# Kernel optimization log

Measured on AMD Instinct MI355X. Metric: run time of the kernel, lower is better.

## Reference

```python
import jax, jax.numpy as jnp
import numpy as np

B, T, L, H = 16, 16, 512, 768


def setup_inputs() -> dict:
    key = jax.random.key(0)
    k1, k2, k3, k4, k5, k6 = jax.random.split(key, 6)
    hn = jax.random.normal(k1, (B, L, H), dtype=jnp.float32)
    decoder_out = jax.random.normal(k2, (B, L, H), dtype=jnp.float32)
    W1 = jax.random.normal(k3, (H, H), dtype=jnp.float32) * (1.0 / np.sqrt(H))
    W2 = jax.random.normal(k4, (H, H), dtype=jnp.float32) * (1.0 / np.sqrt(H))
    V = jax.random.normal(k5, (H,), dtype=jnp.float32) * (1.0 / np.sqrt(H))
    # Ragged, consistent pointer indices: T monotone segment starts per sample,
    # gold boundary Yindex[b,t] in [Xindex[b,t], L).
    step = L // T  # 32
    Xindex = jnp.broadcast_to(jnp.arange(T, dtype=jnp.int64) * step, (B, T))
    offsets = jax.random.randint(k6, (B, T), 0, step, dtype=jnp.int64)
    Yindex = Xindex + offsets
    lens = jnp.full((B,), L, dtype=jnp.int64)
    return {"hn": hn, "decoder_out": decoder_out, "W1": W1, "W2": W2, "V": V,
            "Xindex": Xindex, "Yindex": Yindex, "lens": lens}


def reference(hn, decoder_out, W1, W2, V, Xindex, Yindex, lens):
    # Faithful batched form of training_decoder + pointerLayer:
    #   for each sample i, step j:
    #     en = hn[i, Xindex[i,j]:lens[i]]            (ragged suffix)
    #     dj = decoder_out[i, Yindex[i,j]]           (cur_dj = decoder_out[cur_groundy])
    #     s  = selu(V @ selu(W1 en + W2 dj))
    #     loss += NLL(log_softmax(s), Yindex[i,j]-Xindex[i,j])
    WE = jnp.einsum('blh,gh->blg', hn, W1)                        # [B,L,H]  nnW1(en)
    dj = jnp.take_along_axis(decoder_out, Yindex[:, :, None], axis=1)  # [B,T,H]
    WD = jnp.einsum('bth,gh->btg', dj, W2)                        # [B,T,H]  nnW2(dj)
    act = jax.nn.selu(WE[:, None, :, :] + WD[:, :, None, :])      # [B,T,L,H]
    scores = jax.nn.selu(jnp.einsum('btlh,h->btl', act, V))       # [B,T,L]
    pos = jnp.arange(hn.shape[1])
    mask = (pos[None, None, :] >= Xindex[:, :, None]) & (pos[None, None, :] < lens[:, None, None])
    neg_inf = jnp.finfo(scores.dtype).min
    masked = jnp.where(mask, scores, neg_inf)
    logp = masked - jax.scipy.special.logsumexp(masked, axis=-1, keepdims=True)
    # logits index (Yindex - Xindex) in the sliced array == global index Yindex
    gold = jnp.take_along_axis(logp, Yindex[:, :, None], axis=-1)[..., 0]  # [B,T]
    return -jnp.mean(gold)
```

## Files before the change

kernel.cpp:

```cpp
#include <hip/hip_runtime.h>
#include <hip/hip_bf16.h>
#include <math.h>

#define SELU_SCALE 1.0507009873554805f
#define SELU_ALPHA 1.6732632423543772f

static constexpr int B_ = 16, T_ = 16, L_ = 512, H_ = 768;

typedef __bf16 bf16x8 __attribute__((ext_vector_type(8)));
typedef __bf16 bf16x4 __attribute__((ext_vector_type(4)));
typedef float  f32x4  __attribute__((ext_vector_type(4)));

__device__ __forceinline__ float bf_lo(unsigned u) { return __uint_as_float(u << 16); }
__device__ __forceinline__ float bf_hi(unsigned u) { return __uint_as_float(u & 0xFFFF0000u); }

__device__ __forceinline__ float selu_core(float x) {
    float e = fmaf(__expf(x), SELU_ALPHA, -SELU_ALPHA);
    return x > 0.0f ? x : e;
}

__device__ __forceinline__ bf16x4 cvt4(float4 f) {
    bf16x4 o;
    o.x = (__bf16)f.x; o.y = (__bf16)f.y; o.z = (__bf16)f.z; o.w = (__bf16)f.w;
    return o;
}

__global__ __launch_bounds__(256) void prep_k(
        const float* __restrict__ w1, const float* __restrict__ w2,
        const float* __restrict__ dec, const int* __restrict__ Yi,
        __bf16* __restrict__ w1b, __bf16* __restrict__ w2b,
        float* __restrict__ djf, float* __restrict__ out) {
    const int NW = H_ * H_ / 4;
    int i = blockIdx.x * 256 + threadIdx.x;
    if (i == 0) out[0] = 0.0f;
    if (i < NW) {
        ((bf16x4*)w1b)[i] = cvt4(((const float4*)w1)[i]);
    } else if (i < 2 * NW) {
        int j = i - NW;
        ((bf16x4*)w2b)[j] = cvt4(((const float4*)w2)[j]);
    } else {
        int j = i - 2 * NW;
        int bt = j / 192, c = j % 192;
        int b = bt >> 4;
        int y = Yi[bt];
        ((float4*)djf)[bt * 192 + c] = ((const float4*)dec)[(b * L_ + y) * 192 + c];
    }
}

__device__ __forceinline__ void load16_lds(const __bf16* g, __bf16* l) {
    __builtin_amdgcn_global_load_lds(
        (const __attribute__((address_space(1))) unsigned int*)g,
        (__attribute__((address_space(3))) unsigned int*)l, 16, 0, 0);
}

__global__ __launch_bounds__(256) void gemm_k(
        const float* __restrict__ hn, const float* __restrict__ djf,
        const __bf16* __restrict__ w1b, const __bf16* __restrict__ w2b,
        __bf16* __restrict__ web, __bf16* __restrict__ wdb) {
    __shared__ __bf16 As[64 * 64];
    __shared__ __bf16 Bs[128 * 64];

    int bx = blockIdx.x;
    const float* Af; const __bf16* Bw; __bf16* C;
    if (bx < 768) { Af = hn; Bw = w1b; C = web; }
    else          { bx -= 768; Af = djf; Bw = w2b; C = wdb; }
    const int m0 = (bx / 6) * 64, n0 = (bx % 6) * 128;

    const int wave = threadIdx.x >> 6;
    const int lane = threadIdx.x & 63;
    const int wm = (wave >> 1) * 32, wn = (wave & 1) * 64;
    const int lr = lane & 15, q = lane >> 4;

    const int ar = threadIdx.x >> 2, asp = threadIdx.x & 3;
    const int s0 = (asp * 2)     ^ (ar & 7);
    const int s1 = (asp * 2 + 1) ^ (ar & 7);
    const float* Ag = Af + (size_t)(m0 + ar) * 768 + asp * 16;
    __bf16* Aw0 = &As[ar * 64 + s0 * 8];
    __bf16* Aw1 = &As[ar * 64 + s1 * 8];

    const int brow = wave * 8 + (lane >> 3);
    const int bcol = ((lane & 7) ^ (lane >> 3)) * 8;
    const __bf16* Bg = Bw + (size_t)(n0 + brow) * 768 + bcol;
    __bf16* Bl = &Bs[(wave * 8) * 64];

    int sl[2];
    sl[0] = ((q)     ^ (lr & 7)) * 8;
    sl[1] = ((4 + q) ^ (lr & 7)) * 8;
    int arow_off[2], brow_off[4];
#pragma unroll
    for (int i = 0; i < 2; ++i) arow_off[i] = (wm + i * 16 + lr) * 64;
#pragma unroll
    for (int j = 0; j < 4; ++j) brow_off[j] = (wn + j * 16 + lr) * 64;

    f32x4 acc[2][4] = {};

    for (int k0 = 0; k0 < 768; k0 += 64) {
#pragma unroll
        for (int c = 0; c < 4; ++c)
            load16_lds(Bg + (size_t)c * 32 * 768 + k0, Bl + c * 32 * 64);
        float4 a0 = *(const float4*)(Ag + k0);
        float4 a1 = *(const float4*)(Ag + k0 + 4);
        float4 a2 = *(const float4*)(Ag + k0 + 8);
        float4 a3 = *(const float4*)(Ag + k0 + 12);
        bf16x8 p0, p1;
        p0[0]=(__bf16)a0.x; p0[1]=(__bf16)a0.y; p0[2]=(__bf16)a0.z; p0[3]=(__bf16)a0.w;
        p0[4]=(__bf16)a1.x; p0[5]=(__bf16)a1.y; p0[6]=(__bf16)a1.z; p0[7]=(__bf16)a1.w;
        p1[0]=(__bf16)a2.x; p1[1]=(__bf16)a2.y; p1[2]=(__bf16)a2.z; p1[3]=(__bf16)a2.w;
        p1[4]=(__bf16)a3.x; p1[5]=(__bf16)a3.y; p1[6]=(__bf16)a3.z; p1[7]=(__bf16)a3.w;
        *(bf16x8*)Aw0 = p0;
        *(bf16x8*)Aw1 = p1;
        __syncthreads();

#pragma unroll
        for (int kc = 0; kc < 2; ++kc) {
            bf16x8 af[2], bfr[4];
#pragma unroll
            for (int i = 0; i < 2; ++i) af[i]  = *(const bf16x8*)&As[arow_off[i] + sl[kc]];
#pragma unroll
            for (int j = 0; j < 4; ++j) bfr[j] = *(const bf16x8*)&Bs[brow_off[j] + sl[kc]];
#pragma unroll
            for (int i = 0; i < 2; ++i)
#pragma unroll
                for (int j = 0; j < 4; ++j)
                    acc[i][j] = __builtin_amdgcn_mfma_f32_16x16x32_bf16(af[i], bfr[j], acc[i][j], 0, 0, 0);
        }
        __syncthreads();
    }

#pragma unroll
    for (int i = 0; i < 2; ++i)
#pragma unroll
        for (int j = 0; j < 4; ++j)
#pragma unroll
            for (int r = 0; r < 4; ++r) {
                int row = m0 + wm + i * 16 + q * 4 + r;
                int col = n0 + wn + j * 16 + lr;
                C[(size_t)row * 768 + col] = (__bf16)acc[i][j][r];
            }
}

__global__ __launch_bounds__(256) void scores_k(
        const __bf16* __restrict__ web, const __bf16* __restrict__ wdb,
        const float* __restrict__ V, const int* __restrict__ Xi,
        float* __restrict__ scores) {
    __shared__ float    we_s[16][772];
    __shared__ unsigned wd_s[16][388];
    __shared__ float    v_s[768];

    const int b = blockIdx.x, l0 = blockIdx.y * 16;

    for (int c = threadIdx.x; c < 16 * 96; c += 256) {
        int r = c / 96, cc = c % 96;
        uint4 v = *(const uint4*)(web + ((size_t)(b * L_ + l0 + r)) * H_ + cc * 8);
        float4 f0, f1;
        f0.x = bf_lo(v.x); f0.y = bf_hi(v.x); f0.z = bf_lo(v.y); f0.w = bf_hi(v.y);
        f1.x = bf_lo(v.z); f1.y = bf_hi(v.z); f1.z = bf_lo(v.w); f1.w = bf_hi(v.w);
        *(float4*)&we_s[r][cc * 8]     = f0;
        *(float4*)&we_s[r][cc * 8 + 4] = f1;
    }
    for (int c = threadIdx.x; c < 16 * 96; c += 256) {
        int r = c / 96, cc = c % 96;
        *(uint4*)&wd_s[r][cc * 4] = *(const uint4*)(wdb + ((size_t)(b * T_ + r)) * H_ + cc * 8);
    }
    if (threadIdx.x < 192) *(float4*)&v_s[threadIdx.x * 4] = ((const float4*)V)[threadIdx.x];
    __syncthreads();

    const int t = threadIdx.x >> 4;
    const int ls = threadIdx.x & 15;
    const int l = l0 + ls;
    const int X = Xi[b * T_ + t];
    if (!__any(l >= X)) return;

    float a0 = 0.f, a1 = 0.f, a2 = 0.f, a3 = 0.f;
#pragma unroll 4
    for (int h = 0; h < H_; h += 8) {
        float4 w0 = *(const float4*)&we_s[ls][h];
        float4 w1 = *(const float4*)&we_s[ls][h + 4];
        uint4  wd = *(const uint4*)&wd_s[t][h >> 1];
        float4 v0 = *(const float4*)&v_s[h];
        float4 v1 = *(const float4*)&v_s[h + 4];
        a0 = fmaf(selu_core(w0.x + bf_lo(wd.x)), v0.x, a0);
        a1 = fmaf(selu_core(w0.y + bf_hi(wd.x)), v0.y, a1);
        a2 = fmaf(selu_core(w0.z + bf_lo(wd.y)), v0.z, a2);
        a3 = fmaf(selu_core(w0.w + bf_hi(wd.y)), v0.w, a3);
        a0 = fmaf(selu_core(w1.x + bf_lo(wd.z)), v1.x, a0);
        a1 = fmaf(selu_core(w1.y + bf_hi(wd.z)), v1.y, a1);
        a2 = fmaf(selu_core(w1.z + bf_lo(wd.w)), v1.z, a2);
        a3 = fmaf(selu_core(w1.w + bf_hi(wd.w)), v1.w, a3);
    }
    float dot = SELU_SCALE * ((a0 + a1) + (a2 + a3));
    float sc  = dot > 0.0f ? SELU_SCALE * dot
                           : SELU_SCALE * SELU_ALPHA * (__expf(dot) - 1.0f);
    scores[((size_t)(b * T_ + t)) * L_ + l] = sc;
}

__global__ __launch_bounds__(64) void loss_k(
        const float* __restrict__ scores, const int* __restrict__ Xi,
        const int* __restrict__ Yi, float* __restrict__ out) {
    const int bt = blockIdx.x;
    const int lane = threadIdx.x;
    const int X = Xi[bt];
    const int Y = Yi[bt];
    const float* row = scores + (size_t)bt * L_;

    float m = -INFINITY;
    for (int l = X + lane; l < L_; l += 64) m = fmaxf(m, row[l]);
#pragma unroll
    for (int off = 32; off > 0; off >>= 1) m = fmaxf(m, __shfl_xor(m, off));

    float s = 0.0f;
    for (int l = X + lane; l < L_; l += 64) s += __expf(row[l] - m);
#pragma unroll
    for (int off = 32; off > 0; off >>= 1) s += __shfl_xor(s, off);

    if (lane == 0)
        atomicAdd(out, (m + __logf(s) - row[Y]) * (1.0f / (B_ * T_)));
}

extern "C" void kernel_launch(void* const* d_in, const int* in_sizes, int n_in,
                              void* d_out, int out_size, void* d_ws, size_t ws_size,
                              hipStream_t stream) {
    const float* hn  = (const float*)d_in[0];
    const float* dec = (const float*)d_in[1];
    const float* W1  = (const float*)d_in[2];
    const float* W2  = (const float*)d_in[3];
    const float* V   = (const float*)d_in[4];
    const int*   Xi  = (const int*)d_in[5];
    const int*   Yi  = (const int*)d_in[6];
    float* out = (float*)d_out;

    char* ws = (char*)d_ws;
    size_t off = 0;
    auto alloc = [&](size_t bytes) -> char* {
        char* p = ws + off;
        off += (bytes + 255) & ~(size_t)255;
        return p;
    };
    __bf16* w1b    = (__bf16*)alloc((size_t)H_ * H_ * 2);
    __bf16* w2b    = (__bf16*)alloc((size_t)H_ * H_ * 2);
    float*  djf    = (float*)alloc((size_t)B_ * T_ * H_ * 4);
    __bf16* web    = (__bf16*)alloc((size_t)B_ * L_ * H_ * 2);
    __bf16* wdb    = (__bf16*)alloc((size_t)B_ * T_ * H_ * 2);
    float*  scores = (float*)alloc((size_t)B_ * T_ * L_ * 4);

    prep_k<<<1344, 256, 0, stream>>>(W1, W2, dec, Yi, w1b, w2b, djf, out);

    gemm_k<<<792, 256, 0, stream>>>(hn, djf, w1b, w2b, web, wdb);

    scores_k<<<dim3(B_, L_ / 16), 256, 0, stream>>>(web, wdb, V, Xi, scores);
    loss_k<<<B_ * T_, 64, 0, stream>>>(scores, Xi, Yi, out);
}
```

Before: 163.6 us.

## Fuse WE GEMM with score computation and split WD GEMM into own kernel

The hn·W1 GEMM is fused into the scores kernel. Each 512-thread block computes a 32×768 WE tile with MFMA, parks it in LDS as bf16, and then evaluates the selu/V reduction for all 16 decoder steps. This removes the global round-trip of the full WE intermediate. The small dj·W2 product moves to its own kernel, fed by bf16 dj from prep. The trade-off is only 256 large blocks with about 78KB of LDS each, so occupancy and parallelism drop, and each block streams all of W1.

```diff
diff --git a/kernel.cpp b/kernel.cpp
--- a/kernel.cpp
+++ b/kernel.cpp
@@ -25,11 +25,19 @@
     return o;
 }
 
+__device__ __forceinline__ int sw3(int r) { return (r ^ (r >> 2)) & 3; }
+
+__device__ __forceinline__ void load16_lds(const __bf16* g, __bf16* l) {
+    __builtin_amdgcn_global_load_lds(
+        (const __attribute__((address_space(1))) unsigned int*)g,
+        (__attribute__((address_space(3))) unsigned int*)l, 16, 0, 0);
+}
+
 __global__ __launch_bounds__(256) void prep_k(
         const float* __restrict__ w1, const float* __restrict__ w2,
         const float* __restrict__ dec, const int* __restrict__ Yi,
         __bf16* __restrict__ w1b, __bf16* __restrict__ w2b,
-        float* __restrict__ djf, float* __restrict__ out) {
+        __bf16* __restrict__ djb, float* __restrict__ out) {
     const int NW = H_ * H_ / 4;
     int i = blockIdx.x * 256 + threadIdx.x;
     if (i == 0) out[0] = 0.0f;
@@ -43,155 +51,147 @@
         int bt = j / 192, c = j % 192;
         int b = bt >> 4;
         int y = Yi[bt];
-        ((float4*)djf)[bt * 192 + c] = ((const float4*)dec)[(b * L_ + y) * 192 + c];
-    }
-}
-
-__device__ __forceinline__ void load16_lds(const __bf16* g, __bf16* l) {
-    __builtin_amdgcn_global_load_lds(
-        (const __attribute__((address_space(1))) unsigned int*)g,
-        (__attribute__((address_space(3))) unsigned int*)l, 16, 0, 0);
-}
-
-__global__ __launch_bounds__(256) void gemm_k(
-        const float* __restrict__ hn, const float* __restrict__ djf,
-        const __bf16* __restrict__ w1b, const __bf16* __restrict__ w2b,
-        __bf16* __restrict__ web, __bf16* __restrict__ wdb) {
-    __shared__ __bf16 As[64 * 64];
-    __shared__ __bf16 Bs[128 * 64];
-
-    int bx = blockIdx.x;
-    const float* Af; const __bf16* Bw; __bf16* C;
-    if (bx < 768) { Af = hn; Bw = w1b; C = web; }
-    else          { bx -= 768; Af = djf; Bw = w2b; C = wdb; }
-    const int m0 = (bx / 6) * 64, n0 = (bx % 6) * 128;
-
-    const int wave = threadIdx.x >> 6;
-    const int lane = threadIdx.x & 63;
-    const int wm = (wave >> 1) * 32, wn = (wave & 1) * 64;
+        ((bf16x4*)djb)[bt * 192 + c] = cvt4(((const float4*)dec)[(b * L_ + y) * 192 + c]);
+    }
+}
+
+__global__ __launch_bounds__(256) void wd_k(
+        const __bf16* __restrict__ djb, const __bf16* __restrict__ w2b,
+        __bf16* __restrict__ wdb) {
+    __shared__ __bf16 Bs[128 * 32];
+    __shared__ __bf16 As[16 * 32];
+    const int b = blockIdx.x / 6, n0 = (blockIdx.x % 6) * 128;
+    const int wave = threadIdx.x >> 6, lane = threadIdx.x & 63;
     const int lr = lane & 15, q = lane >> 4;
-
-    const int ar = threadIdx.x >> 2, asp = threadIdx.x & 3;
-    const int s0 = (asp * 2)     ^ (ar & 7);
-    const int s1 = (asp * 2 + 1) ^ (ar & 7);
-    const float* Ag = Af + (size_t)(m0 + ar) * 768 + asp * 16;
-    __bf16* Aw0 = &As[ar * 64 + s0 * 8];
-    __bf16* Aw1 = &As[ar * 64 + s1 * 8];
-
-    const int brow = wave * 8 + (lane >> 3);
-    const int bcol = ((lane & 7) ^ (lane >> 3)) * 8;
-    const __bf16* Bg = Bw + (size_t)(n0 + brow) * 768 + bcol;
-    __bf16* Bl = &Bs[(wave * 8) * 64];
-
-    int sl[2];
-    sl[0] = ((q)     ^ (lr & 7)) * 8;
-    sl[1] = ((4 + q) ^ (lr & 7)) * 8;
-    int arow_off[2], brow_off[4];
-#pragma unroll
-    for (int i = 0; i < 2; ++i) arow_off[i] = (wm + i * 16 + lr) * 64;
-#pragma unroll
-    for (int j = 0; j < 4; ++j) brow_off[j] = (wn + j * 16 + lr) * 64;
-
-    f32x4 acc[2][4] = {};
-
-    for (int k0 = 0; k0 < 768; k0 += 64) {
-#pragma unroll
-        for (int c = 0; c < 4; ++c)
-            load16_lds(Bg + (size_t)c * 32 * 768 + k0, Bl + c * 32 * 64);
-        float4 a0 = *(const float4*)(Ag + k0);
-        float4 a1 = *(const float4*)(Ag + k0 + 4);
-        float4 a2 = *(const float4*)(Ag + k0 + 8);
-        float4 a3 = *(const float4*)(Ag + k0 + 12);
-        bf16x8 p0, p1;
-        p0[0]=(__bf16)a0.x; p0[1]=(__bf16)a0.y; p0[2]=(__bf16)a0.z; p0[3]=(__bf16)a0.w;
-        p0[4]=(__bf16)a1.x; p0[5]=(__bf16)a1.y; p0[6]=(__bf16)a1.z; p0[7]=(__bf16)a1.w;
-        p1[0]=(__bf16)a2.x; p1[1]=(__bf16)a2.y; p1[2]=(__bf16)a2.z; p1[3]=(__bf16)a2.w;
-        p1[4]=(__bf16)a3.x; p1[5]=(__bf16)a3.y; p1[6]=(__bf16)a3.z; p1[7]=(__bf16)a3.w;
-        *(bf16x8*)Aw0 = p0;
-        *(bf16x8*)Aw1 = p1;
-        __syncthreads();
-
-#pragma unroll
-        for (int kc = 0; kc < 2; ++kc) {
-            bf16x8 af[2], bfr[4];
-#pragma unroll
-            for (int i = 0; i < 2; ++i) af[i]  = *(const bf16x8*)&As[arow_off[i] + sl[kc]];
-#pragma unroll
-            for (int j = 0; j < 4; ++j) bfr[j] = *(const bf16x8*)&Bs[brow_off[j] + sl[kc]];
-#pragma unroll
-            for (int i = 0; i < 2; ++i)
-#pragma unroll
-                for (int j = 0; j < 4; ++j)
-                    acc[i][j] = __builtin_amdgcn_mfma_f32_16x16x32_bf16(af[i], bfr[j], acc[i][j], 0, 0, 0);
+    const int dr = lane >> 2;
+    const int segb = ((lane & 3) ^ sw3(dr)) * 8;
+    const __bf16* Bg = w2b + (size_t)(n0 + dr) * 768 + segb;
+    const __bf16* Ag = djb + (size_t)(b * 16 + dr) * 768 + segb;
+    const int rb0 = (wave * 2) * 16, rb1 = (wave * 2 + 1) * 16;
+
+    const int slot = (q ^ sw3(lr)) * 8;
+    const int aoff = lr * 32 + slot;
+    const int boff0 = (wave * 32 + lr) * 32 + slot;
+    const int boff1 = (wave * 32 + 16 + lr) * 32 + slot;
+
+    f32x4 acc0 = {}, acc1 = {};
+    for (int k0 = 0; k0 < 768; k0 += 32) {
+        if (wave == 0) load16_lds(Ag + k0, As);
+        load16_lds(Bg + (size_t)rb0 * 768 + k0, Bs + rb0 * 32);
+        load16_lds(Bg + (size_t)rb1 * 768 + k0, Bs + rb1 * 32);
+        __syncthreads();
+        bf16x8 a  = *(const bf16x8*)&As[aoff];
+        bf16x8 b0 = *(const bf16x8*)&Bs[boff0];
+        bf16x8 b1 = *(const bf16x8*)&Bs[boff1];
+        acc0 = __builtin_amdgcn_mfma_f32_16x16x32_bf16(a, b0, acc0, 0, 0, 0);
+        acc1 = __builtin_amdgcn_mfma_f32_16x16x32_bf16(a, b1, acc1, 0, 0, 0);
+        __syncthreads();
+    }
+#pragma unroll
+    for (int r = 0; r < 4; ++r) {
+        wdb[(size_t)(b * 16 + q * 4 + r) * 768 + n0 + wave * 32 + lr]      = (__bf16)acc0[r];
+        wdb[(size_t)(b * 16 + q * 4 + r) * 768 + n0 + wave * 32 + 16 + lr] = (__bf16)acc1[r];
+    }
+}
+
+__global__ __launch_bounds__(512) void wescore_k(
+        const float* __restrict__ hn, const __bf16* __restrict__ w1b,
+        const __bf16* __restrict__ wdb, const float* __restrict__ V,
+        const int* __restrict__ Xi, float* __restrict__ scores) {
+    __shared__ __align__(16) char smem[79616];
+    __bf16* Bs  = (__bf16*)smem;
+    __bf16* WEs = (__bf16*)smem;
+    __bf16* As  = (__bf16*)(smem + 49664);
+    __bf16* WDs = (__bf16*)(smem + 51712);
+    float*  Vs  = (float*)(smem + 76544);
+
+    const int b = blockIdx.x >> 4, l0 = (blockIdx.x & 15) * 32;
+    const int tid = threadIdx.x;
+    const int wave = tid >> 6, lane = tid & 63;
+    const int lr = lane & 15, q = lane >> 4;
+
+    for (int cid = tid; cid < 16 * 96; cid += 512) {
+        int r = cid / 96, cc = cid % 96;
+        *(uint4*)&WDs[r * 776 + cc * 8] = *(const uint4*)(wdb + (size_t)(b * 16 + r) * 768 + cc * 8);
+    }
+    if (tid < 192) *(float4*)&Vs[tid * 4] = ((const float4*)V)[tid];
+
+    const int dr = lane >> 2;
+    const int segb = ((lane & 3) ^ sw3(dr)) * 8;
+    const __bf16* Bg = w1b + (size_t)dr * 768 + segb;
+
+    const int arow = tid >> 4, apk = tid & 15;
+    const float* Ahn = hn + (size_t)(b * 512 + l0 + arow) * 768 + apk * 2;
+    unsigned* Aw = (unsigned*)&As[arow * 32 + ((apk >> 2) ^ sw3(arow)) * 8 + (apk & 3) * 2];
+
+    const int slot = (q ^ sw3(lr)) * 8;
+    int aoffs[2], boffs[6];
+#pragma unroll
+    for (int i = 0; i < 2; ++i) aoffs[i] = (i * 16 + lr) * 32 + slot;
+#pragma unroll
+    for (int j = 0; j < 6; ++j) boffs[j] = (wave * 96 + j * 16 + lr) * 32 + slot;
+
+    f32x4 acc[2][6] = {};
+
+    for (int k0 = 0; k0 < 768; k0 += 32) {
+#pragma unroll
+        for (int c = 0; c < 6; ++c) {
+            int rb = (c * 8 + wave) * 16;
+            load16_lds(Bg + (size_t)rb * 768 + k0, Bs + rb * 32);
         }
+        float2 av = *(const float2*)(Ahn + k0);
+        union { __bf16 h[2]; unsigned u; } pk;
+        pk.h[0] = (__bf16)av.x; pk.h[1] = (__bf16)av.y;
+        *Aw = pk.u;
+        __syncthreads();
+        bf16x8 af[2], bfr[6];
+#pragma unroll
+        for (int i = 0; i < 2; ++i) af[i]  = *(const bf16x8*)&As[aoffs[i]];
+#pragma unroll
+        for (int j = 0; j < 6; ++j) bfr[j] = *(const bf16x8*)&Bs[boffs[j]];
+#pragma unroll
+        for (int i = 0; i < 2; ++i)
+#pragma unroll
+            for (int j = 0; j < 6; ++j)
+                acc[i][j] = __builtin_amdgcn_mfma_f32_16x16x32_bf16(af[i], bfr[j], acc[i][j], 0, 0, 0);
         __syncthreads();
     }
 
 #pragma unroll
     for (int i = 0; i < 2; ++i)
 #pragma unroll
-        for (int j = 0; j < 4; ++j)
-#pragma unroll
-            for (int r = 0; r < 4; ++r) {
-                int row = m0 + wm + i * 16 + q * 4 + r;
-                int col = n0 + wn + j * 16 + lr;
-                C[(size_t)row * 768 + col] = (__bf16)acc[i][j][r];
-            }
-}
-
-__global__ __launch_bounds__(256) void scores_k(
-        const __bf16* __restrict__ web, const __bf16* __restrict__ wdb,
-        const float* __restrict__ V, const int* __restrict__ Xi,
-        float* __restrict__ scores) {
-    __shared__ float    we_s[16][772];
-    __shared__ unsigned wd_s[16][388];
-    __shared__ float    v_s[768];
-
-    const int b = blockIdx.x, l0 = blockIdx.y * 16;
-
-    for (int c = threadIdx.x; c < 16 * 96; c += 256) {
-        int r = c / 96, cc = c % 96;
-        uint4 v = *(const uint4*)(web + ((size_t)(b * L_ + l0 + r)) * H_ + cc * 8);
-        float4 f0, f1;
-        f0.x = bf_lo(v.x); f0.y = bf_hi(v.x); f0.z = bf_lo(v.y); f0.w = bf_hi(v.y);
-        f1.x = bf_lo(v.z); f1.y = bf_hi(v.z); f1.z = bf_lo(v.w); f1.w = bf_hi(v.w);
-        *(float4*)&we_s[r][cc * 8]     = f0;
-        *(float4*)&we_s[r][cc * 8 + 4] = f1;
-    }
-    for (int c = threadIdx.x; c < 16 * 96; c += 256) {
-        int r = c / 96, cc = c % 96;
-        *(uint4*)&wd_s[r][cc * 4] = *(const uint4*)(wdb + ((size_t)(b * T_ + r)) * H_ + cc * 8);
-    }
-    if (threadIdx.x < 192) *(float4*)&v_s[threadIdx.x * 4] = ((const float4*)V)[threadIdx.x];
+        for (int j = 0; j < 6; ++j)
+#pragma unroll
+            for (int r = 0; r < 4; ++r)
+                WEs[(i * 16 + q * 4 + r) * 776 + wave * 96 + j * 16 + lr] = (__bf16)acc[i][j][r];
     __syncthreads();
 
-    const int t = threadIdx.x >> 4;
-    const int ls = threadIdx.x & 15;
-    const int l = l0 + ls;
-    const int X = Xi[b * T_ + t];
-    if (!__any(l >= X)) return;
+    const int t = tid >> 5, ls = tid & 31, l = l0 + ls;
+    const int X = Xi[b * 16 + t];
+    if (__all(l < X)) return;
 
     float a0 = 0.f, a1 = 0.f, a2 = 0.f, a3 = 0.f;
 #pragma unroll 4
-    for (int h = 0; h < H_; h += 8) {
-        float4 w0 = *(const float4*)&we_s[ls][h];
-        float4 w1 = *(const float4*)&we_s[ls][h + 4];
-        uint4  wd = *(const uint4*)&wd_s[t][h >> 1];
-        float4 v0 = *(const float4*)&v_s[h];
-        float4 v1 = *(const float4*)&v_s[h + 4];
-        a0 = fmaf(selu_core(w0.x + bf_lo(wd.x)), v0.x, a0);
-        a1 = fmaf(selu_core(w0.y + bf_hi(wd.x)), v0.y, a1);
-        a2 = fmaf(selu_core(w0.z + bf_lo(wd.y)), v0.z, a2);
-        a3 = fmaf(selu_core(w0.w + bf_hi(wd.y)), v0.w, a3);
-        a0 = fmaf(selu_core(w1.x + bf_lo(wd.z)), v1.x, a0);
-        a1 = fmaf(selu_core(w1.y + bf_hi(wd.z)), v1.y, a1);
-        a2 = fmaf(selu_core(w1.z + bf_lo(wd.w)), v1.z, a2);
-        a3 = fmaf(selu_core(w1.w + bf_hi(wd.w)), v1.w, a3);
-    }
-    float dot = SELU_SCALE * ((a0 + a1) + (a2 + a3));
-    float sc  = dot > 0.0f ? SELU_SCALE * dot
-                           : SELU_SCALE * SELU_ALPHA * (__expf(dot) - 1.0f);
-    scores[((size_t)(b * T_ + t)) * L_ + l] = sc;
+    for (int h = 0; h < 768; h += 8) {
+        uint4 we = *(const uint4*)&WEs[ls * 776 + h];
+        uint4 wd = *(const uint4*)&WDs[t * 776 + h];
+        float4 v0 = *(const float4*)&Vs[h];
+        float4 v1 = *(const float4*)&Vs[h + 4];
+        a0 = fmaf(selu_core(bf_lo(we.x) + bf_lo(wd.x)), v0.x, a0);
+        a1 = fmaf(selu_core(bf_hi(we.x) + bf_hi(wd.x)), v0.y, a1);
+        a2 = fmaf(selu_core(bf_lo(we.y) + bf_lo(wd.y)), v0.z, a2);
+        a3 = fmaf(selu_core(bf_hi(we.y) + bf_hi(wd.y)), v0.w, a3);
+        a0 = fmaf(selu_core(bf_lo(we.z) + bf_lo(wd.z)), v1.x, a0);
+        a1 = fmaf(selu_core(bf_hi(we.z) + bf_hi(wd.z)), v1.y, a1);
+        a2 = fmaf(selu_core(bf_lo(we.w) + bf_lo(wd.w)), v1.z, a2);
+        a3 = fmaf(selu_core(bf_hi(we.w) + bf_hi(wd.w)), v1.w, a3);
+    }
+    if (l >= X) {
+        float dot = SELU_SCALE * ((a0 + a1) + (a2 + a3));
+        float sc  = dot > 0.0f ? SELU_SCALE * dot
+                               : SELU_SCALE * SELU_ALPHA * (__expf(dot) - 1.0f);
+        scores[(size_t)(b * 16 + t) * 512 + l] = sc;
+    }
 }
 
 __global__ __launch_bounds__(64) void loss_k(
@@ -238,15 +238,12 @@
     };
     __bf16* w1b    = (__bf16*)alloc((size_t)H_ * H_ * 2);
     __bf16* w2b    = (__bf16*)alloc((size_t)H_ * H_ * 2);
-    float*  djf    = (float*)alloc((size_t)B_ * T_ * H_ * 4);
-    __bf16* web    = (__bf16*)alloc((size_t)B_ * L_ * H_ * 2);
+    __bf16* djb    = (__bf16*)alloc((size_t)B_ * T_ * H_ * 2);
     __bf16* wdb    = (__bf16*)alloc((size_t)B_ * T_ * H_ * 2);
     float*  scores = (float*)alloc((size_t)B_ * T_ * L_ * 4);
 
-    prep_k<<<1344, 256, 0, stream>>>(W1, W2, dec, Yi, w1b, w2b, djf, out);
-
-    gemm_k<<<792, 256, 0, stream>>>(hn, djf, w1b, w2b, web, wdb);
-
-    scores_k<<<dim3(B_, L_ / 16), 256, 0, stream>>>(web, wdb, V, Xi, scores);
+    prep_k<<<1344, 256, 0, stream>>>(W1, W2, dec, Yi, w1b, w2b, djb, out);
+    wd_k<<<96, 256, 0, stream>>>(djb, w2b, wdb);
+    wescore_k<<<256, 512, 0, stream>>>(hn, w1b, wdb, V, Xi, scores);
     loss_k<<<B_ * T_, 64, 0, stream>>>(scores, Xi, Yi, out);
 }
```

Result: slower. 172.0 us (+5.1%).

## Register-prefetch next K tile in GEMM with smaller BK and new swizzle

Applied to the files above, without the earlier changes.

The GEMM main loop changes from BK=64 with direct global-to-LDS loads for B to BK=32. Both A and B are now prefetched into registers one iteration ahead, so global latency overlaps with the MFMA work, and the LDS swizzle is redesigned for 32-wide rows. This halves LDS use, which can raise occupancy. The cost is twice as many barriers per K, more register pressure, and loss of the async LDS-load path.

```diff
diff --git a/kernel.cpp b/kernel.cpp
--- a/kernel.cpp
+++ b/kernel.cpp
@@ -24,6 +24,8 @@
     o.x = (__bf16)f.x; o.y = (__bf16)f.y; o.z = (__bf16)f.z; o.w = (__bf16)f.w;
     return o;
 }
+
+__device__ __forceinline__ int xsw(int r) { return (r >> 1) & 3; }
 
 __global__ __launch_bounds__(256) void prep_k(
         const float* __restrict__ w1, const float* __restrict__ w2,
@@ -47,18 +49,12 @@
     }
 }
 
-__device__ __forceinline__ void load16_lds(const __bf16* g, __bf16* l) {
-    __builtin_amdgcn_global_load_lds(
-        (const __attribute__((address_space(1))) unsigned int*)g,
-        (__attribute__((address_space(3))) unsigned int*)l, 16, 0, 0);
-}
-
 __global__ __launch_bounds__(256) void gemm_k(
         const float* __restrict__ hn, const float* __restrict__ djf,
         const __bf16* __restrict__ w1b, const __bf16* __restrict__ w2b,
         __bf16* __restrict__ web, __bf16* __restrict__ wdb) {
-    __shared__ __bf16 As[64 * 64];
-    __shared__ __bf16 Bs[128 * 64];
+    __shared__ __bf16 As[64 * 32];
+    __shared__ __bf16 Bs[128 * 32];
 
     int bx = blockIdx.x;
     const float* Af; const __bf16* Bw; __bf16* C;
@@ -66,65 +62,68 @@
     else          { bx -= 768; Af = djf; Bw = w2b; C = wdb; }
     const int m0 = (bx / 6) * 64, n0 = (bx % 6) * 128;
 
-    const int wave = threadIdx.x >> 6;
-    const int lane = threadIdx.x & 63;
+    const int tid = threadIdx.x;
+    const int wave = tid >> 6, lane = tid & 63;
     const int wm = (wave >> 1) * 32, wn = (wave & 1) * 64;
     const int lr = lane & 15, q = lane >> 4;
 
-    const int ar = threadIdx.x >> 2, asp = threadIdx.x & 3;
-    const int s0 = (asp * 2)     ^ (ar & 7);
-    const int s1 = (asp * 2 + 1) ^ (ar & 7);
-    const float* Ag = Af + (size_t)(m0 + ar) * 768 + asp * 16;
-    __bf16* Aw0 = &As[ar * 64 + s0 * 8];
-    __bf16* Aw1 = &As[ar * 64 + s1 * 8];
-
-    const int brow = wave * 8 + (lane >> 3);
-    const int bcol = ((lane & 7) ^ (lane >> 3)) * 8;
-    const __bf16* Bg = Bw + (size_t)(n0 + brow) * 768 + bcol;
-    __bf16* Bl = &Bs[(wave * 8) * 64];
-
-    int sl[2];
-    sl[0] = ((q)     ^ (lr & 7)) * 8;
-    sl[1] = ((4 + q) ^ (lr & 7)) * 8;
-    int arow_off[2], brow_off[4];
-#pragma unroll
-    for (int i = 0; i < 2; ++i) arow_off[i] = (wm + i * 16 + lr) * 64;
-#pragma unroll
-    for (int j = 0; j < 4; ++j) brow_off[j] = (wn + j * 16 + lr) * 64;
+    const int arow = tid >> 2, aseg = tid & 3;
+    const float* Ag = Af + (size_t)(m0 + arow) * 768 + aseg * 8;
+    bf16x8* AsW = (bf16x8*)&As[arow * 32 + ((aseg ^ xsw(arow)) * 8)];
+
+    const int brow = tid >> 1, bs0 = (tid & 1) * 2;
+    const __bf16* Bg = Bw + (size_t)(n0 + brow) * 768 + bs0 * 8;
+    uint4* BsW0 = (uint4*)&Bs[brow * 32 + (((bs0)     ^ xsw(brow)) * 8)];
+    uint4* BsW1 = (uint4*)&Bs[brow * 32 + (((bs0 + 1) ^ xsw(brow)) * 8)];
+
+    int aoff[2], boff[4];
+#pragma unroll
+    for (int i = 0; i < 2; ++i) {
+        int r = wm + i * 16 + lr;
+        aoff[i] = r * 32 + (q ^ xsw(r)) * 8;
+    }
+#pragma unroll
+    for (int j = 0; j < 4; ++j) {
+        int r = wn + j * 16 + lr;
+        boff[j] = r * 32 + (q ^ xsw(r)) * 8;
+    }
 
     f32x4 acc[2][4] = {};
 
-    for (int k0 = 0; k0 < 768; k0 += 64) {
-#pragma unroll
-        for (int c = 0; c < 4; ++c)
-            load16_lds(Bg + (size_t)c * 32 * 768 + k0, Bl + c * 32 * 64);
-        float4 a0 = *(const float4*)(Ag + k0);
-        float4 a1 = *(const float4*)(Ag + k0 + 4);
-        float4 a2 = *(const float4*)(Ag + k0 + 8);
-        float4 a3 = *(const float4*)(Ag + k0 + 12);
-        bf16x8 p0, p1;
-        p0[0]=(__bf16)a0.x; p0[1]=(__bf16)a0.y; p0[2]=(__bf16)a0.z; p0[3]=(__bf16)a0.w;
-        p0[4]=(__bf16)a1.x; p0[5]=(__bf16)a1.y; p0[6]=(__bf16)a1.z; p0[7]=(__bf16)a1.w;
-        p1[0]=(__bf16)a2.x; p1[1]=(__bf16)a2.y; p1[2]=(__bf16)a2.z; p1[3]=(__bf16)a2.w;
-        p1[4]=(__bf16)a3.x; p1[5]=(__bf16)a3.y; p1[6]=(__bf16)a3.z; p1[7]=(__bf16)a3.w;
-        *(bf16x8*)Aw0 = p0;
-        *(bf16x8*)Aw1 = p1;
-        __syncthreads();
-
-#pragma unroll
-        for (int kc = 0; kc < 2; ++kc) {
-            bf16x8 af[2], bfr[4];
-#pragma unroll
-            for (int i = 0; i < 2; ++i) af[i]  = *(const bf16x8*)&As[arow_off[i] + sl[kc]];
-#pragma unroll
-            for (int j = 0; j < 4; ++j) bfr[j] = *(const bf16x8*)&Bs[brow_off[j] + sl[kc]];
-#pragma unroll
-            for (int i = 0; i < 2; ++i)
-#pragma unroll
-                for (int j = 0; j < 4; ++j)
-                    acc[i][j] = __builtin_amdgcn_mfma_f32_16x16x32_bf16(af[i], bfr[j], acc[i][j], 0, 0, 0);
+    float4 pa0 = *(const float4*)(Ag);
+    float4 pa1 = *(const float4*)(Ag + 4);
+    uint4  pb0 = *(const uint4*)(Bg);
+    uint4  pb1 = *(const uint4*)(Bg + 8);
+
+    for (int k0 = 0; k0 < 768; k0 += 32) {
+        bf16x8 aw;
+        aw[0] = (__bf16)pa0.x; aw[1] = (__bf16)pa0.y;
+        aw[2] = (__bf16)pa0.z; aw[3] = (__bf16)pa0.w;
+        aw[4] = (__bf16)pa1.x; aw[5] = (__bf16)pa1.y;
+        aw[6] = (__bf16)pa1.z; aw[7] = (__bf16)pa1.w;
+        *AsW  = aw;
+        *BsW0 = pb0;
+        *BsW1 = pb1;
+        asm volatile("s_waitcnt lgkmcnt(0)\n\ts_barrier" ::: "memory");
+
+        if (k0 + 32 < 768) {
+            pa0 = *(const float4*)(Ag + k0 + 32);
+            pa1 = *(const float4*)(Ag + k0 + 36);
+            pb0 = *(const uint4*)(Bg + k0 + 32);
+            pb1 = *(const uint4*)(Bg + k0 + 40);
         }
-        __syncthreads();
+
+        bf16x8 af[2], bfr[4];
+#pragma unroll
+        for (int i = 0; i < 2; ++i) af[i]  = *(const bf16x8*)&As[aoff[i]];
+#pragma unroll
+        for (int j = 0; j < 4; ++j) bfr[j] = *(const bf16x8*)&Bs[boff[j]];
+#pragma unroll
+        for (int i = 0; i < 2; ++i)
+#pragma unroll
+            for (int j = 0; j < 4; ++j)
+                acc[i][j] = __builtin_amdgcn_mfma_f32_16x16x32_bf16(af[i], bfr[j], acc[i][j], 0, 0, 0);
+        asm volatile("s_barrier" ::: "memory");
     }
 
 #pragma unroll
@@ -244,9 +243,7 @@
     float*  scores = (float*)alloc((size_t)B_ * T_ * L_ * 4);
 
     prep_k<<<1344, 256, 0, stream>>>(W1, W2, dec, Yi, w1b, w2b, djf, out);
-
     gemm_k<<<792, 256, 0, stream>>>(hn, djf, w1b, w2b, web, wdb);
-
     scores_k<<<dim3(B_, L_ / 16), 256, 0, stream>>>(web, wdb, V, Xi, scores);
     loss_k<<<B_ * T_, 64, 0, stream>>>(scores, Xi, Yi, out);
 }
```

Result: no change. 165.8 us (+1.4%).
